# Kernel tuning notes

Measured on AMD Instinct MI355X. Metric: run time of the kernel, lower is better.

## Reference

```python
import jax, jax.numpy as jnp
import numpy as np

B, S, D, H = 4, 2048, 1024, 16
DH = D // H


def setup_inputs() -> dict:
    key = jax.random.key(0)
    k1, k2, k3, k4, k5 = jax.random.split(key, 5)
    X = jax.random.normal(k1, (B, S, D), dtype=jnp.float32)
    W1 = jax.random.normal(k2, (3 * D, D), dtype=jnp.float32) * 0.02
    b1 = jax.random.normal(k3, (3 * D,), dtype=jnp.float32) * 0.01
    W2 = jax.random.normal(k4, (D, D), dtype=jnp.float32) * 0.02
    b2 = jax.random.normal(k5, (D,), dtype=jnp.float32) * 0.01
    return {"X": X, "W1": W1, "b1": b1, "W2": W2, "b2": b2}


def reference(X, W1, b1, W2, b2):
    b, s, d = X.shape
    # fused QKV projection (nn.Linear: y = x @ W.T + b)
    Y = X @ W1.T + b1                                   # [B,S,3D]
    Q, K, V = jnp.split(Y, 3, axis=2)                   # each [B,S,D]
    # reshape(x): view (B,S,H,DH) then permute(0,2,3,1) -> [B,H,DH,S]
    q = Q.reshape(b, s, H, DH).transpose(0, 2, 3, 1)    # [B,H,DH,S]
    v = V.reshape(b, s, H, DH).transpose(0, 2, 3, 1)    # [B,H,DH,S]
    # reshape(x, k=True): permute(0,2,1,3) -> [B,H,S,DH]
    k = K.reshape(b, s, H, DH).transpose(0, 2, 1, 3)    # [B,H,S,DH]
    # w = q @ k / sqrt(q.size(-1)) ; note q.size(-1) == S in this layout
    w = jnp.einsum('bhds,bhse->bhde', q, k) / jnp.sqrt(jnp.asarray(s, X.dtype))  # [B,H,DH,DH]
    w = jax.nn.softmax(w, axis=-1)
    out = jnp.einsum('bhde,bhes->bhds', w, v)           # [B,H,DH,S]
    # cat(): raw contiguous view of [B,H,DH,S] into [B,S,H*DH] (memory-order reshape)
    out = out.reshape(b, s, H * DH)                     # [B,S,D]
    return out @ W2.T + b2
```

## Files before the change

kernel.cpp:

```cpp
#include <hip/hip_runtime.h>
#include <stdint.h>

#define B_ 4
#define S_ 2048
#define D_ 1024
#define H_ 16
#define DH_ 64
#define M_TOT (B_*S_)
#define N1_ (3*D_)
#define K_ D_
#define NCH 8

typedef __bf16 bf16_8 __attribute__((ext_vector_type(8)));
typedef float  f32x4  __attribute__((ext_vector_type(4)));
typedef unsigned short u16;

typedef __attribute__((address_space(1))) const void* gas_t;
typedef __attribute__((address_space(3))) void*       las_t;

__device__ __forceinline__ unsigned short f2bf(float f) {
    union { float f; unsigned u; } v; v.f = f;
    unsigned r = v.u + 0x7FFFu + ((v.u >> 16) & 1u);
    return (unsigned short)(r >> 16);
}

__device__ __forceinline__ void async_ld16(const void* g, void* l) {
    __builtin_amdgcn_global_load_lds((gas_t)g, (las_t)l, 16, 0, 0);
}

__global__ __launch_bounds__(256)
void cast_kernel(const float* __restrict__ X, const float* __restrict__ W1,
                 const float* __restrict__ W2, unsigned short* __restrict__ Xb,
                 unsigned short* __restrict__ W1b, unsigned short* __restrict__ W2b) {
    const int nX  = (M_TOT * K_) / 4;
    const int nW1 = (N1_ * K_) / 4;
    int i = blockIdx.x * 256 + threadIdx.x;
    const float4* src; unsigned short* dst; int j;
    if (i < nX)            { src = (const float4*)X;  dst = Xb;  j = i; }
    else if (i < nX + nW1) { src = (const float4*)W1; dst = W1b; j = i - nX; }
    else                   { src = (const float4*)W2; dst = W2b; j = i - nX - nW1; }
    float4 v = src[j];
    ushort4 o;
    o.x = f2bf(v.x); o.y = f2bf(v.y); o.z = f2bf(v.z); o.w = f2bf(v.w);
    ((ushort4*)dst)[j] = o;
}

template<int N, int NBX, int EPI>
__global__ __launch_bounds__(256)
void gemm_bt(const unsigned short* __restrict__ A,
             const unsigned short* __restrict__ Bm,
             const float* __restrict__ bias,
             void* __restrict__ C, int K,
             u16* __restrict__ QT, u16* __restrict__ KT, u16* __restrict__ Vb) {
    __shared__ unsigned short As[128 * 64];
    __shared__ unsigned short Bs[128 * 64];
    const int t    = threadIdx.x;
    const int wid  = t >> 6;
    const int lane = t & 63;
    const int lrow = lane & 15;
    const int lq   = lane >> 4;

    const int lid  = blockIdx.y * NBX + blockIdx.x;
    const int xcd  = lid & 7;
    const int slot = lid >> 3;
    const int by   = xcd * (gridDim.y >> 3) + slot / NBX;
    const int bx   = slot % NBX;
    const int m0   = by * 128;
    const int n0   = bx * 128;

    const int wm   = (wid >> 1) * 64;
    const int wn   = (wid & 1) * 64;

    f32x4 acc[4][4] = {};

    for (int k0 = 0; k0 < K; k0 += 64) {
#pragma unroll
        for (int p = 0; p < 4; p++) {
            const int c   = p * 256 + t;
            const int row = c >> 3;
            const int kb  = (c & 7) ^ (row & 7);
            async_ld16(A  + (size_t)(m0 + row) * K + k0 + kb * 8, (char*)As + c * 16);
            async_ld16(Bm + (size_t)(n0 + row) * K + k0 + kb * 8, (char*)Bs + c * 16);
        }
        __syncthreads();

#pragma unroll
        for (int ks = 0; ks < 2; ks++) {
            bf16_8 af[4], bfr[4];
#pragma unroll
            for (int mt = 0; mt < 4; mt++) {
                const int r  = wm + mt * 16 + lrow;
                const int kb = (ks * 4 + lq) ^ (r & 7);
                af[mt] = *(const bf16_8*)(As + (r * 8 + kb) * 8);
            }
#pragma unroll
            for (int nt = 0; nt < 4; nt++) {
                const int r  = wn + nt * 16 + lrow;
                const int kb = (ks * 4 + lq) ^ (r & 7);
                bfr[nt] = *(const bf16_8*)(Bs + (r * 8 + kb) * 8);
            }
#pragma unroll
            for (int mt = 0; mt < 4; mt++)
#pragma unroll
                for (int nt = 0; nt < 4; nt++)
                    acc[mt][nt] = __builtin_amdgcn_mfma_f32_16x16x32_bf16(af[mt], bfr[nt], acc[mt][nt], 0, 0, 0);
        }
        __syncthreads();
    }

#pragma unroll
    for (int nt = 0; nt < 4; nt++) {
        const int col = n0 + wn + nt * 16 + lrow;
        const float bv = bias[col];
#pragma unroll
        for (int mt = 0; mt < 4; mt++) {
            const int row = m0 + wm + mt * 16 + lq * 4;
            f32x4 a = acc[mt][nt];
            if constexpr (EPI == 2) {
                ushort4 o;
                o.x = f2bf(a[0] + bv); o.y = f2bf(a[1] + bv);
                o.z = f2bf(a[2] + bv); o.w = f2bf(a[3] + bv);
                const int b = row >> 11, s = row & 2047;
                const int d = col & 63;
                if (col < 1024) {
                    *(ushort4*)(QT + ((size_t)(b * 16 + (col >> 6)) * 64 + d) * (size_t)S_ + s) = o;
                } else if (col < 2048) {
                    *(ushort4*)(KT + ((size_t)(b * 16 + ((col >> 6) - 16)) * 64 + d) * (size_t)S_ + s) = o;
                } else {
                    u16* vp = Vb + ((size_t)b * S_ + s) * (size_t)D_ + (col - 2048);
                    vp[0]      = o.x;
                    vp[D_]     = o.y;
                    vp[2 * D_] = o.z;
                    vp[3 * D_] = o.w;
                }
            } else {
                float* Cp = (float*)C;
#pragma unroll
                for (int i = 0; i < 4; i++)
                    Cp[(size_t)(row + i) * N + col] = a[i] + bv;
            }
        }
    }
}

__global__ __launch_bounds__(256)
void attn_scores_t(const u16* __restrict__ QT, const u16* __restrict__ KT,
                   float* __restrict__ Scp) {
    const int bh = blockIdx.x, ch = blockIdx.y;
    const int t = threadIdx.x, wid = t >> 6, lane = t & 63;
    const int lrow = lane & 15, lq = lane >> 4;

    const u16* Qh = QT + (size_t)bh * 64 * S_;
    const u16* Kh = KT + (size_t)bh * 64 * S_;

    f32x4 acc[4] = {};
    const int sbeg = ch * (S_ / NCH);
#pragma unroll 2
    for (int s0 = sbeg; s0 < sbeg + S_ / NCH; s0 += 32) {
        const int so = s0 + lq * 8;
        bf16_8 aq = *(const bf16_8*)(Qh + (wid * 16 + lrow) * S_ + so);
        bf16_8 bk0 = *(const bf16_8*)(Kh + ( 0 + lrow) * S_ + so);
        bf16_8 bk1 = *(const bf16_8*)(Kh + (16 + lrow) * S_ + so);
        bf16_8 bk2 = *(const bf16_8*)(Kh + (32 + lrow) * S_ + so);
        bf16_8 bk3 = *(const bf16_8*)(Kh + (48 + lrow) * S_ + so);
        acc[0] = __builtin_amdgcn_mfma_f32_16x16x32_bf16(aq, bk0, acc[0], 0, 0, 0);
        acc[1] = __builtin_amdgcn_mfma_f32_16x16x32_bf16(aq, bk1, acc[1], 0, 0, 0);
        acc[2] = __builtin_amdgcn_mfma_f32_16x16x32_bf16(aq, bk2, acc[2], 0, 0, 0);
        acc[3] = __builtin_amdgcn_mfma_f32_16x16x32_bf16(aq, bk3, acc[3], 0, 0, 0);
    }

    float* out = Scp + (size_t)(bh * NCH + ch) * 64 * 64;
#pragma unroll
    for (int nt = 0; nt < 4; nt++)
#pragma unroll
        for (int i = 0; i < 4; i++)
            out[(wid * 16 + lq * 4 + i) * 64 + nt * 16 + lrow] = acc[nt][i];
}

__global__ __launch_bounds__(256)
void attn_out_fused(const unsigned short* __restrict__ Vb,
                    const float* __restrict__ Scp,
                    unsigned short* __restrict__ O) {
    __shared__ unsigned short Ws[64 * 72];
    const int bh = blockIdx.x, sc = blockIdx.y;
    const int b = bh >> 4, h = bh & 15;
    const size_t vbase = (size_t)b * S_ * D_;
    const int voff = h * 64;
    const int t = threadIdx.x, wid = t >> 6, lane = t & 63;
    const int lrow = lane & 15, lq = lane >> 4;

    {
        const int d = t >> 2, q = t & 3;
        float s[16] = {};
#pragma unroll
        for (int c = 0; c < NCH; c++) {
            const float4* p = (const float4*)(Scp + ((size_t)(bh * NCH + c) * 64 + d) * 64 + q * 16);
#pragma unroll
            for (int j = 0; j < 4; j++) {
                float4 v = p[j];
                s[j*4+0] += v.x; s[j*4+1] += v.y; s[j*4+2] += v.z; s[j*4+3] += v.w;
            }
        }
        const float scale = 0.022097086912079608f;
        float m = -3.0e38f;
#pragma unroll
        for (int i = 0; i < 16; i++) { s[i] *= scale; m = fmaxf(m, s[i]); }
        m = fmaxf(m, __shfl_xor(m, 1));
        m = fmaxf(m, __shfl_xor(m, 2));
        float sum = 0.f;
#pragma unroll
        for (int i = 0; i < 16; i++) { s[i] = __expf(s[i] - m); sum += s[i]; }
        sum += __shfl_xor(sum, 1);
        sum += __shfl_xor(sum, 2);
        const float inv = 1.0f / sum;
        unsigned short* w = Ws + d * 72 + q * 16;
#pragma unroll
        for (int i = 0; i < 16; i++) w[i] = f2bf(s[i] * inv);
    }
    __syncthreads();

    bf16_8 aw[4][2];
#pragma unroll
    for (int mt = 0; mt < 4; mt++)
#pragma unroll
        for (int ks = 0; ks < 2; ks++)
            aw[mt][ks] = *(const bf16_8*)(Ws + (mt * 16 + lrow) * 72 + ks * 32 + lq * 8);

    const size_t obase = (size_t)b * (H_ * DH_ * S_) + (size_t)h * (DH_ * S_);
    const int s0 = sc * 256 + wid * 64;
    f32x4 o[4][4] = {};
#pragma unroll
    for (int ks = 0; ks < 2; ks++) {
        bf16_8 bv[4];
#pragma unroll
        for (int nt = 0; nt < 4; nt++)
            bv[nt] = *(const bf16_8*)(Vb + vbase + (size_t)(s0 + nt * 16 + lrow) * D_ + voff + ks * 32 + lq * 8);
#pragma unroll
        for (int mt = 0; mt < 4; mt++)
#pragma unroll
            for (int nt = 0; nt < 4; nt++)
                o[mt][nt] = __builtin_amdgcn_mfma_f32_16x16x32_bf16(aw[mt][ks], bv[nt], o[mt][nt], 0, 0, 0);
    }
#pragma unroll
    for (int mt = 0; mt < 4; mt++)
#pragma unroll
        for (int nt = 0; nt < 4; nt++) {
            const int d = mt * 16 + lq * 4;
            const int s = s0 + nt * 16 + lrow;
#pragma unroll
            for (int i = 0; i < 4; i++)
                O[obase + (size_t)(d + i) * S_ + s] = f2bf(o[mt][nt][i]);
        }
}

extern "C" void kernel_launch(void* const* d_in, const int* in_sizes, int n_in,
                              void* d_out, int out_size, void* d_ws, size_t ws_size,
                              hipStream_t stream) {
    const float* X  = (const float*)d_in[0];
    const float* W1 = (const float*)d_in[1];
    const float* b1 = (const float*)d_in[2];
    const float* W2 = (const float*)d_in[3];
    const float* b2 = (const float*)d_in[4];

    char* ws = (char*)d_ws;
    unsigned short* Xb  = (unsigned short*)(ws + 0);
    unsigned short* W1b = (unsigned short*)(ws + (16u << 20));
    unsigned short* W2b = (unsigned short*)(ws + (22u << 20));
    unsigned short* QT  = (unsigned short*)(ws + (24u << 20));
    unsigned short* KT  = (unsigned short*)(ws + (40u << 20));
    unsigned short* Vb  = (unsigned short*)(ws + (56u << 20));
    unsigned short* Ob  = (unsigned short*)(ws + (1u << 20));
    float* Scp = (float*)d_out;

    cast_kernel<<<12288, 256, 0, stream>>>(X, W1, W2, Xb, W1b, W2b);
    gemm_bt<N1_, N1_/128, 2><<<dim3(N1_ / 128, M_TOT / 128), 256, 0, stream>>>(
        Xb, W1b, b1, nullptr, K_, QT, KT, Vb);
    attn_scores_t<<<dim3(64, NCH), 256, 0, stream>>>(QT, KT, Scp);
    attn_out_fused<<<dim3(64, NCH), 256, 0, stream>>>(Vb, Scp, Ob);
    gemm_bt<D_, D_/128, 0><<<dim3(D_ / 128, M_TOT / 128), 256, 0, stream>>>(
        Ob, W2b, b2, d_out, K_, nullptr, nullptr, nullptr);
}
```

Baseline: 213.8 us.

## Fuse attention score and output kernels into one per-head block

Merges the partial-score kernel and the softmax+PV kernel into a single kernel with one 512-thread block per (batch, head). Each wave computes partial QK^T over a sequence chunk and stores it in LDS, then the block reduces the partials, applies softmax and performs the PV product. This removes one launch and the global-memory round trip of partial scores. In exchange it uses about 148 KB of LDS per block and only 64 blocks, which leaves most CUs idle.

```diff
diff --git a/kernel.cpp b/kernel.cpp
--- a/kernel.cpp
+++ b/kernel.cpp
@@ -9,7 +9,6 @@
 #define M_TOT (B_*S_)
 #define N1_ (3*D_)
 #define K_ D_
-#define NCH 8
 
 typedef __bf16 bf16_8 __attribute__((ext_vector_type(8)));
 typedef float  f32x4  __attribute__((ext_vector_type(4)));
@@ -143,114 +142,115 @@
     }
 }
 
-__global__ __launch_bounds__(256)
-void attn_scores_t(const u16* __restrict__ QT, const u16* __restrict__ KT,
-                   float* __restrict__ Scp) {
-    const int bh = blockIdx.x, ch = blockIdx.y;
+__global__ __launch_bounds__(512)
+void attn_head(const u16* __restrict__ QT, const u16* __restrict__ KT,
+               const u16* __restrict__ Vb, u16* __restrict__ O) {
+    __shared__ float Sp[8][64 * 68];
+    __shared__ u16   Ws[64 * 72];
+    const int bh = blockIdx.x;
+    const int b = bh >> 4, h = bh & 15;
     const int t = threadIdx.x, wid = t >> 6, lane = t & 63;
     const int lrow = lane & 15, lq = lane >> 4;
 
     const u16* Qh = QT + (size_t)bh * 64 * S_;
     const u16* Kh = KT + (size_t)bh * 64 * S_;
 
-    f32x4 acc[4] = {};
-    const int sbeg = ch * (S_ / NCH);
+    {
+        f32x4 acc[4][4] = {};
+        const int sbeg = wid * 256;
 #pragma unroll 2
-    for (int s0 = sbeg; s0 < sbeg + S_ / NCH; s0 += 32) {
-        const int so = s0 + lq * 8;
-        bf16_8 aq = *(const bf16_8*)(Qh + (wid * 16 + lrow) * S_ + so);
-        bf16_8 bk0 = *(const bf16_8*)(Kh + ( 0 + lrow) * S_ + so);
-        bf16_8 bk1 = *(const bf16_8*)(Kh + (16 + lrow) * S_ + so);
-        bf16_8 bk2 = *(const bf16_8*)(Kh + (32 + lrow) * S_ + so);
-        bf16_8 bk3 = *(const bf16_8*)(Kh + (48 + lrow) * S_ + so);
-        acc[0] = __builtin_amdgcn_mfma_f32_16x16x32_bf16(aq, bk0, acc[0], 0, 0, 0);
-        acc[1] = __builtin_amdgcn_mfma_f32_16x16x32_bf16(aq, bk1, acc[1], 0, 0, 0);
-        acc[2] = __builtin_amdgcn_mfma_f32_16x16x32_bf16(aq, bk2, acc[2], 0, 0, 0);
-        acc[3] = __builtin_amdgcn_mfma_f32_16x16x32_bf16(aq, bk3, acc[3], 0, 0, 0);
-    }
-
-    float* out = Scp + (size_t)(bh * NCH + ch) * 64 * 64;
-#pragma unroll
-    for (int nt = 0; nt < 4; nt++)
-#pragma unroll
-        for (int i = 0; i < 4; i++)
-            out[(wid * 16 + lq * 4 + i) * 64 + nt * 16 + lrow] = acc[nt][i];
-}
-
-__global__ __launch_bounds__(256)
-void attn_out_fused(const unsigned short* __restrict__ Vb,
-                    const float* __restrict__ Scp,
-                    unsigned short* __restrict__ O) {
-    __shared__ unsigned short Ws[64 * 72];
-    const int bh = blockIdx.x, sc = blockIdx.y;
-    const int b = bh >> 4, h = bh & 15;
+        for (int s0 = sbeg; s0 < sbeg + 256; s0 += 32) {
+            const int so = s0 + lq * 8;
+            bf16_8 aq[4], bk[4];
+#pragma unroll
+            for (int mt = 0; mt < 4; mt++)
+                aq[mt] = *(const bf16_8*)(Qh + (mt * 16 + lrow) * S_ + so);
+#pragma unroll
+            for (int nt = 0; nt < 4; nt++)
+                bk[nt] = *(const bf16_8*)(Kh + (nt * 16 + lrow) * S_ + so);
+#pragma unroll
+            for (int mt = 0; mt < 4; mt++)
+#pragma unroll
+                for (int nt = 0; nt < 4; nt++)
+                    acc[mt][nt] = __builtin_amdgcn_mfma_f32_16x16x32_bf16(aq[mt], bk[nt], acc[mt][nt], 0, 0, 0);
+        }
+        float* myp = &Sp[wid][0];
+#pragma unroll
+        for (int mt = 0; mt < 4; mt++)
+#pragma unroll
+            for (int nt = 0; nt < 4; nt++)
+#pragma unroll
+                for (int i = 0; i < 4; i++)
+                    myp[(mt * 16 + lq * 4 + i) * 68 + nt * 16 + lrow] = acc[mt][nt][i];
+    }
+    __syncthreads();
+
+    {
+        const int d = t >> 3, q = t & 7;
+        float s[8] = {};
+#pragma unroll
+        for (int c = 0; c < 8; c++) {
+            const float* p = &Sp[c][d * 68 + q * 8];
+#pragma unroll
+            for (int j = 0; j < 8; j++) s[j] += p[j];
+        }
+        const float scale = 0.022097086912079608f;
+        float m = -3.0e38f;
+#pragma unroll
+        for (int i = 0; i < 8; i++) { s[i] *= scale; m = fmaxf(m, s[i]); }
+        m = fmaxf(m, __shfl_xor(m, 1));
+        m = fmaxf(m, __shfl_xor(m, 2));
+        m = fmaxf(m, __shfl_xor(m, 4));
+        float sum = 0.f;
+#pragma unroll
+        for (int i = 0; i < 8; i++) { s[i] = __expf(s[i] - m); sum += s[i]; }
+        sum += __shfl_xor(sum, 1);
+        sum += __shfl_xor(sum, 2);
+        sum += __shfl_xor(sum, 4);
+        const float inv = 1.0f / sum;
+        u16* w = Ws + d * 72 + q * 8;
+#pragma unroll
+        for (int i = 0; i < 8; i++) w[i] = f2bf(s[i] * inv);
+    }
+    __syncthreads();
+
+    bf16_8 aw[4][2];
+#pragma unroll
+    for (int mt = 0; mt < 4; mt++)
+#pragma unroll
+        for (int ks = 0; ks < 2; ks++)
+            aw[mt][ks] = *(const bf16_8*)(Ws + (mt * 16 + lrow) * 72 + ks * 32 + lq * 8);
+
     const size_t vbase = (size_t)b * S_ * D_;
     const int voff = h * 64;
-    const int t = threadIdx.x, wid = t >> 6, lane = t & 63;
-    const int lrow = lane & 15, lq = lane >> 4;
-
-    {
-        const int d = t >> 2, q = t & 3;
-        float s[16] = {};
-#pragma unroll
-        for (int c = 0; c < NCH; c++) {
-            const float4* p = (const float4*)(Scp + ((size_t)(bh * NCH + c) * 64 + d) * 64 + q * 16);
-#pragma unroll
-            for (int j = 0; j < 4; j++) {
-                float4 v = p[j];
-                s[j*4+0] += v.x; s[j*4+1] += v.y; s[j*4+2] += v.z; s[j*4+3] += v.w;
-            }
-        }
-        const float scale = 0.022097086912079608f;
-        float m = -3.0e38f;
-#pragma unroll
-        for (int i = 0; i < 16; i++) { s[i] *= scale; m = fmaxf(m, s[i]); }
-        m = fmaxf(m, __shfl_xor(m, 1));
-        m = fmaxf(m, __shfl_xor(m, 2));
-        float sum = 0.f;
-#pragma unroll
-        for (int i = 0; i < 16; i++) { s[i] = __expf(s[i] - m); sum += s[i]; }
-        sum += __shfl_xor(sum, 1);
-        sum += __shfl_xor(sum, 2);
-        const float inv = 1.0f / sum;
-        unsigned short* w = Ws + d * 72 + q * 16;
-#pragma unroll
-        for (int i = 0; i < 16; i++) w[i] = f2bf(s[i] * inv);
-    }
-    __syncthreads();
-
-    bf16_8 aw[4][2];
-#pragma unroll
-    for (int mt = 0; mt < 4; mt++)
-#pragma unroll
-        for (int ks = 0; ks < 2; ks++)
-            aw[mt][ks] = *(const bf16_8*)(Ws + (mt * 16 + lrow) * 72 + ks * 32 + lq * 8);
-
     const size_t obase = (size_t)b * (H_ * DH_ * S_) + (size_t)h * (DH_ * S_);
-    const int s0 = sc * 256 + wid * 64;
-    f32x4 o[4][4] = {};
-#pragma unroll
-    for (int ks = 0; ks < 2; ks++) {
-        bf16_8 bv[4];
-#pragma unroll
-        for (int nt = 0; nt < 4; nt++)
-            bv[nt] = *(const bf16_8*)(Vb + vbase + (size_t)(s0 + nt * 16 + lrow) * D_ + voff + ks * 32 + lq * 8);
+#pragma unroll
+    for (int sb = 0; sb < 4; sb++) {
+        const int s0 = wid * 256 + sb * 64;
+        f32x4 o[4][4] = {};
+#pragma unroll
+        for (int ks = 0; ks < 2; ks++) {
+            bf16_8 bv[4];
+#pragma unroll
+            for (int nt = 0; nt < 4; nt++)
+                bv[nt] = *(const bf16_8*)(Vb + vbase + (size_t)(s0 + nt * 16 + lrow) * D_ + voff + ks * 32 + lq * 8);
+#pragma unroll
+            for (int mt = 0; mt < 4; mt++)
+#pragma unroll
+                for (int nt = 0; nt < 4; nt++)
+                    o[mt][nt] = __builtin_amdgcn_mfma_f32_16x16x32_bf16(aw[mt][ks], bv[nt], o[mt][nt], 0, 0, 0);
+        }
 #pragma unroll
         for (int mt = 0; mt < 4; mt++)
 #pragma unroll
-            for (int nt = 0; nt < 4; nt++)
-                o[mt][nt] = __builtin_amdgcn_mfma_f32_16x16x32_bf16(aw[mt][ks], bv[nt], o[mt][nt], 0, 0, 0);
-    }
-#pragma unroll
-    for (int mt = 0; mt < 4; mt++)
-#pragma unroll
-        for (int nt = 0; nt < 4; nt++) {
-            const int d = mt * 16 + lq * 4;
-            const int s = s0 + nt * 16 + lrow;
-#pragma unroll
-            for (int i = 0; i < 4; i++)
-                O[obase + (size_t)(d + i) * S_ + s] = f2bf(o[mt][nt][i]);
-        }
+            for (int nt = 0; nt < 4; nt++) {
+                const int d = mt * 16 + lq * 4;
+                const int s = s0 + nt * 16 + lrow;
+#pragma unroll
+                for (int i = 0; i < 4; i++)
+                    O[obase + (size_t)(d + i) * S_ + s] = f2bf(o[mt][nt][i]);
+            }
+    }
 }
 
 extern "C" void kernel_launch(void* const* d_in, const int* in_sizes, int n_in,
@@ -270,13 +270,11 @@
     unsigned short* KT  = (unsigned short*)(ws + (40u << 20));
     unsigned short* Vb  = (unsigned short*)(ws + (56u << 20));
     unsigned short* Ob  = (unsigned short*)(ws + (1u << 20));
-    float* Scp = (float*)d_out;
 
     cast_kernel<<<12288, 256, 0, stream>>>(X, W1, W2, Xb, W1b, W2b);
     gemm_bt<N1_, N1_/128, 2><<<dim3(N1_ / 128, M_TOT / 128), 256, 0, stream>>>(
         Xb, W1b, b1, nullptr, K_, QT, KT, Vb);
-    attn_scores_t<<<dim3(64, NCH), 256, 0, stream>>>(QT, KT, Scp);
-    attn_out_fused<<<dim3(64, NCH), 256, 0, stream>>>(Vb, Scp, Ob);
+    attn_head<<<64, 512, 0, stream>>>(QT, KT, Vb, Ob);
     gemm_bt<D_, D_/128, 0><<<dim3(D_ / 128, M_TOT / 128), 256, 0, stream>>>(
         Ob, W2b, b2, d_out, K_, nullptr, nullptr, nullptr);
 }
```

Result: slower. 219.2 us (+2.5%).

## Reassociate attention output with W2: project V by W2 before applying softmax weights

Applied to the files above, without the earlier changes.

Uses associativity so that V (stored transposed) is multiplied by W2 first in a full-size GEMM, and a small per-head GEMM then applies the 64x64 softmax weights and adds the bias. This removes the separate attention-output kernel and the round trip of the O intermediate, replacing them with a standalone softmax kernel and a light GEMM. The QK score kernel is also rewritten to stage tiles through LDS with swizzling, and V is now written transposed with vector stores. The cost is an extra bf16 rounding of the VW product and more complex index mapping, which risks layout mistakes.

```diff
diff --git a/kernel.cpp b/kernel.cpp
--- a/kernel.cpp
+++ b/kernel.cpp
@@ -51,7 +51,7 @@
              const unsigned short* __restrict__ Bm,
              const float* __restrict__ bias,
              void* __restrict__ C, int K,
-             u16* __restrict__ QT, u16* __restrict__ KT, u16* __restrict__ Vb) {
+             u16* __restrict__ QT, u16* __restrict__ KT, u16* __restrict__ VT) {
     __shared__ unsigned short As[128 * 64];
     __shared__ unsigned short Bs[128 * 64];
     const int t    = threadIdx.x;
@@ -68,6 +68,11 @@
     const int m0   = by * 128;
     const int n0   = bx * 128;
 
+    const int inst  = by >> 3;
+    const int hblk  = by & 7;
+    const size_t arow0 = (size_t)((inst >> 1) * 1024 + hblk * 128);
+    const int koff  = (inst & 1) * 1024;
+
     const int wm   = (wid >> 1) * 64;
     const int wn   = (wid & 1) * 64;
 
@@ -79,7 +84,10 @@
             const int c   = p * 256 + t;
             const int row = c >> 3;
             const int kb  = (c & 7) ^ (row & 7);
-            async_ld16(A  + (size_t)(m0 + row) * K + k0 + kb * 8, (char*)As + c * 16);
+            if constexpr (EPI == 3)
+                async_ld16(A + (arow0 + row) * (size_t)S_ + koff + k0 + kb * 8, (char*)As + c * 16);
+            else
+                async_ld16(A + (size_t)(m0 + row) * K + k0 + kb * 8, (char*)As + c * 16);
             async_ld16(Bm + (size_t)(n0 + row) * K + k0 + kb * 8, (char*)Bs + c * 16);
         }
         __syncthreads();
@@ -111,7 +119,7 @@
 #pragma unroll
     for (int nt = 0; nt < 4; nt++) {
         const int col = n0 + wn + nt * 16 + lrow;
-        const float bv = bias[col];
+        const float bv = (EPI == 2) ? bias[col] : 0.f;
 #pragma unroll
         for (int mt = 0; mt < 4; mt++) {
             const int row = m0 + wm + mt * 16 + lq * 4;
@@ -127,130 +135,181 @@
                 } else if (col < 2048) {
                     *(ushort4*)(KT + ((size_t)(b * 16 + ((col >> 6) - 16)) * 64 + d) * (size_t)S_ + s) = o;
                 } else {
-                    u16* vp = Vb + ((size_t)b * S_ + s) * (size_t)D_ + (col - 2048);
-                    vp[0]      = o.x;
-                    vp[D_]     = o.y;
-                    vp[2 * D_] = o.z;
-                    vp[3 * D_] = o.w;
+                    *(ushort4*)(VT + ((size_t)(b * 16 + ((col >> 6) - 32)) * 64 + d) * (size_t)S_ + s) = o;
                 }
             } else {
-                float* Cp = (float*)C;
-#pragma unroll
-                for (int i = 0; i < 4; i++)
-                    Cp[(size_t)(row + i) * N + col] = a[i] + bv;
-            }
-        }
-    }
-}
-
-__global__ __launch_bounds__(256)
-void attn_scores_t(const u16* __restrict__ QT, const u16* __restrict__ KT,
-                   float* __restrict__ Scp) {
+                ushort4 o;
+                o.x = f2bf(a[0]); o.y = f2bf(a[1]); o.z = f2bf(a[2]); o.w = f2bf(a[3]);
+                u16* Cp = (u16*)C;
+                *(ushort4*)(Cp + ((size_t)((row >> 10) * 16 + ((row >> 6) & 15)) * 1024 + col) * 64
+                                + (row & 63)) = o;
+            }
+        }
+    }
+}
+
+__global__ __launch_bounds__(256)
+void attn_qk(const u16* __restrict__ QT, const u16* __restrict__ KT,
+             float* __restrict__ Scp) {
+    __shared__ u16 Qs[64 * 64];
+    __shared__ u16 Ks[64 * 64];
     const int bh = blockIdx.x, ch = blockIdx.y;
     const int t = threadIdx.x, wid = t >> 6, lane = t & 63;
     const int lrow = lane & 15, lq = lane >> 4;
-
+    const int wm2 = (wid >> 1) * 32, wn2 = (wid & 1) * 32;
     const u16* Qh = QT + (size_t)bh * 64 * S_;
     const u16* Kh = KT + (size_t)bh * 64 * S_;
 
-    f32x4 acc[4] = {};
-    const int sbeg = ch * (S_ / NCH);
-#pragma unroll 2
-    for (int s0 = sbeg; s0 < sbeg + S_ / NCH; s0 += 32) {
-        const int so = s0 + lq * 8;
-        bf16_8 aq = *(const bf16_8*)(Qh + (wid * 16 + lrow) * S_ + so);
-        bf16_8 bk0 = *(const bf16_8*)(Kh + ( 0 + lrow) * S_ + so);
-        bf16_8 bk1 = *(const bf16_8*)(Kh + (16 + lrow) * S_ + so);
-        bf16_8 bk2 = *(const bf16_8*)(Kh + (32 + lrow) * S_ + so);
-        bf16_8 bk3 = *(const bf16_8*)(Kh + (48 + lrow) * S_ + so);
-        acc[0] = __builtin_amdgcn_mfma_f32_16x16x32_bf16(aq, bk0, acc[0], 0, 0, 0);
-        acc[1] = __builtin_amdgcn_mfma_f32_16x16x32_bf16(aq, bk1, acc[1], 0, 0, 0);
-        acc[2] = __builtin_amdgcn_mfma_f32_16x16x32_bf16(aq, bk2, acc[2], 0, 0, 0);
-        acc[3] = __builtin_amdgcn_mfma_f32_16x16x32_bf16(aq, bk3, acc[3], 0, 0, 0);
-    }
-
-    float* out = Scp + (size_t)(bh * NCH + ch) * 64 * 64;
-#pragma unroll
-    for (int nt = 0; nt < 4; nt++)
-#pragma unroll
-        for (int i = 0; i < 4; i++)
-            out[(wid * 16 + lq * 4 + i) * 64 + nt * 16 + lrow] = acc[nt][i];
-}
-
-__global__ __launch_bounds__(256)
-void attn_out_fused(const unsigned short* __restrict__ Vb,
-                    const float* __restrict__ Scp,
-                    unsigned short* __restrict__ O) {
-    __shared__ unsigned short Ws[64 * 72];
-    const int bh = blockIdx.x, sc = blockIdx.y;
-    const int b = bh >> 4, h = bh & 15;
-    const size_t vbase = (size_t)b * S_ * D_;
-    const int voff = h * 64;
+    f32x4 acc[2][2] = {};
+    for (int kt = 0; kt < 4; kt++) {
+        const int s0 = ch * 256 + kt * 64;
+#pragma unroll
+        for (int p = 0; p < 4; p++) {
+            const int c   = p * 256 + t;
+            const int cc  = c & 511;
+            const int row = cc >> 3;
+            const int kb  = (cc & 7) ^ (row & 7);
+            if (p < 2)
+                async_ld16(Qh + (size_t)row * S_ + s0 + kb * 8, (char*)Qs + cc * 16);
+            else
+                async_ld16(Kh + (size_t)row * S_ + s0 + kb * 8, (char*)Ks + cc * 16);
+        }
+        __syncthreads();
+#pragma unroll
+        for (int ks = 0; ks < 2; ks++) {
+            bf16_8 aq[2], bk[2];
+#pragma unroll
+            for (int mt = 0; mt < 2; mt++) {
+                const int r  = wm2 + mt * 16 + lrow;
+                const int kb = (ks * 4 + lq) ^ (r & 7);
+                aq[mt] = *(const bf16_8*)(Qs + (r * 8 + kb) * 8);
+            }
+#pragma unroll
+            for (int nt = 0; nt < 2; nt++) {
+                const int r  = wn2 + nt * 16 + lrow;
+                const int kb = (ks * 4 + lq) ^ (r & 7);
+                bk[nt] = *(const bf16_8*)(Ks + (r * 8 + kb) * 8);
+            }
+#pragma unroll
+            for (int mt = 0; mt < 2; mt++)
+#pragma unroll
+                for (int nt = 0; nt < 2; nt++)
+                    acc[mt][nt] = __builtin_amdgcn_mfma_f32_16x16x32_bf16(aq[mt], bk[nt], acc[mt][nt], 0, 0, 0);
+        }
+        __syncthreads();
+    }
+
+    float* out = Scp + (size_t)(bh * NCH + ch) * 4096;
+#pragma unroll
+    for (int mt = 0; mt < 2; mt++)
+#pragma unroll
+        for (int nt = 0; nt < 2; nt++)
+#pragma unroll
+            for (int i = 0; i < 4; i++)
+                out[(wm2 + mt * 16 + lq * 4 + i) * 64 + wn2 + nt * 16 + lrow] = acc[mt][nt][i];
+}
+
+__global__ __launch_bounds__(256)
+void attn_softmax(const float* __restrict__ Scp, unsigned short* __restrict__ Wb) {
+    const int bh = blockIdx.x;
+    const int t = threadIdx.x;
+    const int d = t >> 2, q = t & 3;
+    float s[16] = {};
+#pragma unroll
+    for (int c = 0; c < NCH; c++) {
+        const float4* p = (const float4*)(Scp + ((size_t)(bh * NCH + c) * 64 + d) * 64 + q * 16);
+#pragma unroll
+        for (int j = 0; j < 4; j++) {
+            float4 v = p[j];
+            s[j*4+0] += v.x; s[j*4+1] += v.y; s[j*4+2] += v.z; s[j*4+3] += v.w;
+        }
+    }
+    const float scale = 0.022097086912079608f;
+    float m = -3.0e38f;
+#pragma unroll
+    for (int i = 0; i < 16; i++) { s[i] *= scale; m = fmaxf(m, s[i]); }
+    m = fmaxf(m, __shfl_xor(m, 1));
+    m = fmaxf(m, __shfl_xor(m, 2));
+    float sum = 0.f;
+#pragma unroll
+    for (int i = 0; i < 16; i++) { s[i] = __expf(s[i] - m); sum += s[i]; }
+    sum += __shfl_xor(sum, 1);
+    sum += __shfl_xor(sum, 2);
+    const float inv = 1.0f / sum;
+    unsigned short* w = Wb + (size_t)bh * 4096 + d * 64 + q * 16;
+    ushort4 o0, o1, o2, o3;
+    o0.x=f2bf(s[0]*inv);  o0.y=f2bf(s[1]*inv);  o0.z=f2bf(s[2]*inv);  o0.w=f2bf(s[3]*inv);
+    o1.x=f2bf(s[4]*inv);  o1.y=f2bf(s[5]*inv);  o1.z=f2bf(s[6]*inv);  o1.w=f2bf(s[7]*inv);
+    o2.x=f2bf(s[8]*inv);  o2.y=f2bf(s[9]*inv);  o2.z=f2bf(s[10]*inv); o2.w=f2bf(s[11]*inv);
+    o3.x=f2bf(s[12]*inv); o3.y=f2bf(s[13]*inv); o3.z=f2bf(s[14]*inv); o3.w=f2bf(s[15]*inv);
+    ((ushort4*)w)[0]=o0; ((ushort4*)w)[1]=o1; ((ushort4*)w)[2]=o2; ((ushort4*)w)[3]=o3;
+}
+
+__global__ __launch_bounds__(256)
+void gemm_light(const u16* __restrict__ Wb, const u16* __restrict__ VWT,
+                const float* __restrict__ b2, float* __restrict__ out) {
+    __shared__ u16 Ws[64 * 64];
+    __shared__ u16 Vs[256 * 64];
+    const int bx = blockIdx.x, byy = blockIdx.y;
+    const int n0 = bx * 128;
+    const int b = byy >> 4, h = byy & 15;
     const int t = threadIdx.x, wid = t >> 6, lane = t & 63;
     const int lrow = lane & 15, lq = lane >> 4;
-
-    {
-        const int d = t >> 2, q = t & 3;
-        float s[16] = {};
-#pragma unroll
-        for (int c = 0; c < NCH; c++) {
-            const float4* p = (const float4*)(Scp + ((size_t)(bh * NCH + c) * 64 + d) * 64 + q * 16);
-#pragma unroll
-            for (int j = 0; j < 4; j++) {
-                float4 v = p[j];
-                s[j*4+0] += v.x; s[j*4+1] += v.y; s[j*4+2] += v.z; s[j*4+3] += v.w;
-            }
-        }
-        const float scale = 0.022097086912079608f;
-        float m = -3.0e38f;
-#pragma unroll
-        for (int i = 0; i < 16; i++) { s[i] *= scale; m = fmaxf(m, s[i]); }
-        m = fmaxf(m, __shfl_xor(m, 1));
-        m = fmaxf(m, __shfl_xor(m, 2));
-        float sum = 0.f;
-#pragma unroll
-        for (int i = 0; i < 16; i++) { s[i] = __expf(s[i] - m); sum += s[i]; }
-        sum += __shfl_xor(sum, 1);
-        sum += __shfl_xor(sum, 2);
-        const float inv = 1.0f / sum;
-        unsigned short* w = Ws + d * 72 + q * 16;
-#pragma unroll
-        for (int i = 0; i < 16; i++) w[i] = f2bf(s[i] * inv);
+    const int wsl = wid >> 1;
+    const int wn  = wid & 1;
+
+#pragma unroll
+    for (int j = 0; j < 2; j++) {
+        const int c = j * 256 + t;
+        const int row = c >> 3, kb = (c & 7) ^ (row & 7);
+        async_ld16(Wb + (size_t)byy * 4096 + row * 64 + kb * 8, (char*)Ws + c * 16);
+    }
+#pragma unroll
+    for (int p = 0; p < 8; p++) {
+        const int c = p * 256 + t;
+        const int slice = c >> 10, rowc = (c >> 3) & 127;
+        const int kb = (c & 7) ^ (rowc & 7);
+        async_ld16(VWT + ((size_t)((b * 2 + slice) * 16 + h) * 1024 + n0 + rowc) * 64 + kb * 8,
+                   (char*)Vs + c * 16);
     }
     __syncthreads();
 
-    bf16_8 aw[4][2];
-#pragma unroll
-    for (int mt = 0; mt < 4; mt++)
-#pragma unroll
-        for (int ks = 0; ks < 2; ks++)
-            aw[mt][ks] = *(const bf16_8*)(Ws + (mt * 16 + lrow) * 72 + ks * 32 + lq * 8);
-
-    const size_t obase = (size_t)b * (H_ * DH_ * S_) + (size_t)h * (DH_ * S_);
-    const int s0 = sc * 256 + wid * 64;
-    f32x4 o[4][4] = {};
+    f32x4 acc[4][4] = {};
 #pragma unroll
     for (int ks = 0; ks < 2; ks++) {
-        bf16_8 bv[4];
-#pragma unroll
-        for (int nt = 0; nt < 4; nt++)
-            bv[nt] = *(const bf16_8*)(Vb + vbase + (size_t)(s0 + nt * 16 + lrow) * D_ + voff + ks * 32 + lq * 8);
+        bf16_8 af[4], bfr[4];
+#pragma unroll
+        for (int mt = 0; mt < 4; mt++) {
+            const int r  = mt * 16 + lrow;
+            const int kb = (ks * 4 + lq) ^ (r & 7);
+            af[mt] = *(const bf16_8*)(Ws + (r * 8 + kb) * 8);
+        }
+#pragma unroll
+        for (int nt = 0; nt < 4; nt++) {
+            const int rn = wn * 64 + nt * 16 + lrow;
+            const int kb = (ks * 4 + lq) ^ (rn & 7);
+            bfr[nt] = *(const bf16_8*)(Vs + ((wsl * 128 + rn) * 8 + kb) * 8);
+        }
 #pragma unroll
         for (int mt = 0; mt < 4; mt++)
 #pragma unroll
             for (int nt = 0; nt < 4; nt++)
-                o[mt][nt] = __builtin_amdgcn_mfma_f32_16x16x32_bf16(aw[mt][ks], bv[nt], o[mt][nt], 0, 0, 0);
-    }
-#pragma unroll
-    for (int mt = 0; mt < 4; mt++)
-#pragma unroll
-        for (int nt = 0; nt < 4; nt++) {
-            const int d = mt * 16 + lq * 4;
-            const int s = s0 + nt * 16 + lrow;
-#pragma unroll
-            for (int i = 0; i < 4; i++)
-                O[obase + (size_t)(d + i) * S_ + s] = f2bf(o[mt][nt][i]);
-        }
+                acc[mt][nt] = __builtin_amdgcn_mfma_f32_16x16x32_bf16(af[mt], bfr[nt], acc[mt][nt], 0, 0, 0);
+    }
+
+    float* op = out + (size_t)byy * 128 * 1024;
+#pragma unroll
+    for (int nt = 0; nt < 4; nt++) {
+        const int col = n0 + wn * 64 + nt * 16 + lrow;
+        const float bv = b2[col];
+#pragma unroll
+        for (int mt = 0; mt < 4; mt++)
+#pragma unroll
+            for (int i = 0; i < 4; i++) {
+                const int d = mt * 16 + lq * 4 + i;
+                op[(size_t)(2 * d + wsl) * 1024 + col] = acc[mt][nt][i] + bv;
+            }
+    }
 }
 
 extern "C" void kernel_launch(void* const* d_in, const int* in_sizes, int n_in,
@@ -268,15 +327,17 @@
     unsigned short* W2b = (unsigned short*)(ws + (22u << 20));
     unsigned short* QT  = (unsigned short*)(ws + (24u << 20));
     unsigned short* KT  = (unsigned short*)(ws + (40u << 20));
-    unsigned short* Vb  = (unsigned short*)(ws + (56u << 20));
-    unsigned short* Ob  = (unsigned short*)(ws + (1u << 20));
+    unsigned short* VT  = (unsigned short*)(ws + (56u << 20));
+    unsigned short* Wb  = (unsigned short*)(ws + 0);
+    unsigned short* VWT = (unsigned short*)(ws + (1u << 20));
     float* Scp = (float*)d_out;
 
     cast_kernel<<<12288, 256, 0, stream>>>(X, W1, W2, Xb, W1b, W2b);
     gemm_bt<N1_, N1_/128, 2><<<dim3(N1_ / 128, M_TOT / 128), 256, 0, stream>>>(
-        Xb, W1b, b1, nullptr, K_, QT, KT, Vb);
-    attn_scores_t<<<dim3(64, NCH), 256, 0, stream>>>(QT, KT, Scp);
-    attn_out_fused<<<dim3(64, NCH), 256, 0, stream>>>(Vb, Scp, Ob);
-    gemm_bt<D_, D_/128, 0><<<dim3(D_ / 128, M_TOT / 128), 256, 0, stream>>>(
-        Ob, W2b, b2, d_out, K_, nullptr, nullptr, nullptr);
-}
+        Xb, W1b, b1, nullptr, K_, QT, KT, VT);
+    attn_qk<<<dim3(64, NCH), 256, 0, stream>>>(QT, KT, Scp);
+    attn_softmax<<<64, 256, 0, stream>>>(Scp, Wb);
+    gemm_bt<D_, D_/128, 3><<<dim3(D_ / 128, M_TOT / 128), 256, 0, stream>>>(
+        VT, W2b, b2, VWT, K_, nullptr, nullptr, nullptr);
+    gemm_light<<<dim3(8, 64), 256, 0, stream>>>(Wb, VWT, b2, (float*)d_out);
+}
```

After: 217.2 us. Within noise of the previous version (+1.6%).

## Stage Q/K tiles in swizzled LDS for QK scores with 2x2 warp tiling

Applied to the files above, without the earlier changes.

The QK^T partial-score kernel now loads 64x64 Q and K tiles into shared memory with async 16-byte loads and an XOR swizzle. Each wave then computes a 32x32 output block from LDS instead of having every wave re-read all of K from global memory. The intent is to cut redundant global/L2 traffic and get better-coalesced loads. The cost is two barriers per k-tile with no double buffering, on a kernel that is small relative to the GEMMs.

```diff
diff --git a/kernel.cpp b/kernel.cpp
--- a/kernel.cpp
+++ b/kernel.cpp
@@ -144,37 +144,64 @@
 }
 
 __global__ __launch_bounds__(256)
-void attn_scores_t(const u16* __restrict__ QT, const u16* __restrict__ KT,
-                   float* __restrict__ Scp) {
+void attn_qk(const u16* __restrict__ QT, const u16* __restrict__ KT,
+             float* __restrict__ Scp) {
+    __shared__ u16 Qs[64 * 64];
+    __shared__ u16 Ks[64 * 64];
     const int bh = blockIdx.x, ch = blockIdx.y;
     const int t = threadIdx.x, wid = t >> 6, lane = t & 63;
     const int lrow = lane & 15, lq = lane >> 4;
-
+    const int wm2 = (wid >> 1) * 32, wn2 = (wid & 1) * 32;
     const u16* Qh = QT + (size_t)bh * 64 * S_;
     const u16* Kh = KT + (size_t)bh * 64 * S_;
 
-    f32x4 acc[4] = {};
-    const int sbeg = ch * (S_ / NCH);
-#pragma unroll 2
-    for (int s0 = sbeg; s0 < sbeg + S_ / NCH; s0 += 32) {
-        const int so = s0 + lq * 8;
-        bf16_8 aq = *(const bf16_8*)(Qh + (wid * 16 + lrow) * S_ + so);
-        bf16_8 bk0 = *(const bf16_8*)(Kh + ( 0 + lrow) * S_ + so);
-        bf16_8 bk1 = *(const bf16_8*)(Kh + (16 + lrow) * S_ + so);
-        bf16_8 bk2 = *(const bf16_8*)(Kh + (32 + lrow) * S_ + so);
-        bf16_8 bk3 = *(const bf16_8*)(Kh + (48 + lrow) * S_ + so);
-        acc[0] = __builtin_amdgcn_mfma_f32_16x16x32_bf16(aq, bk0, acc[0], 0, 0, 0);
-        acc[1] = __builtin_amdgcn_mfma_f32_16x16x32_bf16(aq, bk1, acc[1], 0, 0, 0);
-        acc[2] = __builtin_amdgcn_mfma_f32_16x16x32_bf16(aq, bk2, acc[2], 0, 0, 0);
-        acc[3] = __builtin_amdgcn_mfma_f32_16x16x32_bf16(aq, bk3, acc[3], 0, 0, 0);
-    }
-
-    float* out = Scp + (size_t)(bh * NCH + ch) * 64 * 64;
-#pragma unroll
-    for (int nt = 0; nt < 4; nt++)
-#pragma unroll
-        for (int i = 0; i < 4; i++)
-            out[(wid * 16 + lq * 4 + i) * 64 + nt * 16 + lrow] = acc[nt][i];
+    f32x4 acc[2][2] = {};
+    for (int kt = 0; kt < 4; kt++) {
+        const int s0 = ch * 256 + kt * 64;
+#pragma unroll
+        for (int p = 0; p < 4; p++) {
+            const int c   = p * 256 + t;
+            const int cc  = c & 511;
+            const int row = cc >> 3;
+            const int kb  = (cc & 7) ^ (row & 7);
+            if (p < 2)
+                async_ld16(Qh + (size_t)row * S_ + s0 + kb * 8, (char*)Qs + cc * 16);
+            else
+                async_ld16(Kh + (size_t)row * S_ + s0 + kb * 8, (char*)Ks + cc * 16);
+        }
+        __syncthreads();
+#pragma unroll
+        for (int ks = 0; ks < 2; ks++) {
+            bf16_8 aq[2], bk[2];
+#pragma unroll
+            for (int mt = 0; mt < 2; mt++) {
+                const int r  = wm2 + mt * 16 + lrow;
+                const int kb = (ks * 4 + lq) ^ (r & 7);
+                aq[mt] = *(const bf16_8*)(Qs + (r * 8 + kb) * 8);
+            }
+#pragma unroll
+            for (int nt = 0; nt < 2; nt++) {
+                const int r  = wn2 + nt * 16 + lrow;
+                const int kb = (ks * 4 + lq) ^ (r & 7);
+                bk[nt] = *(const bf16_8*)(Ks + (r * 8 + kb) * 8);
+            }
+#pragma unroll
+            for (int mt = 0; mt < 2; mt++)
+#pragma unroll
+                for (int nt = 0; nt < 2; nt++)
+                    acc[mt][nt] = __builtin_amdgcn_mfma_f32_16x16x32_bf16(aq[mt], bk[nt], acc[mt][nt], 0, 0, 0);
+        }
+        __syncthreads();
+    }
+
+    float* out = Scp + (size_t)(bh * NCH + ch) * 4096;
+#pragma unroll
+    for (int mt = 0; mt < 2; mt++)
+#pragma unroll
+        for (int nt = 0; nt < 2; nt++)
+#pragma unroll
+            for (int i = 0; i < 4; i++)
+                out[(wm2 + mt * 16 + lq * 4 + i) * 64 + wn2 + nt * 16 + lrow] = acc[mt][nt][i];
 }
 
 __global__ __launch_bounds__(256)
@@ -275,7 +302,7 @@
     cast_kernel<<<12288, 256, 0, stream>>>(X, W1, W2, Xb, W1b, W2b);
     gemm_bt<N1_, N1_/128, 2><<<dim3(N1_ / 128, M_TOT / 128), 256, 0, stream>>>(
         Xb, W1b, b1, nullptr, K_, QT, KT, Vb);
-    attn_scores_t<<<dim3(64, NCH), 256, 0, stream>>>(QT, KT, Scp);
+    attn_qk<<<dim3(64, NCH), 256, 0, stream>>>(QT, KT, Scp);
     attn_out_fused<<<dim3(64, NCH), 256, 0, stream>>>(Vb, Scp, Ob);
     gemm_bt<D_, D_/128, 0><<<dim3(D_ / 128, M_TOT / 128), 256, 0, stream>>>(
         Ob, W2b, b2, d_out, K_, nullptr, nullptr, nullptr);
```

Measured after the change: 200.0 us. -6.5%, faster.
